# Optimization experiments

Measured on AMD Instinct MI355X. Metric: run time of the kernel, lower is better.

The kernel has to match this reference:

```python
import jax, jax.numpy as jnp
import numpy as np

EPS = 1e-5  # BatchNorm eps (eval mode, running stats mean=0, var=1)
BN_SCALE = 1.0 / np.sqrt(1.0 + EPS)


def setup_inputs() -> dict:
    key = jax.random.key(0)
    ks = jax.random.split(key, 5)
    N, T, C, V, K = 64, 300, 64, 25, 3
    x = jax.random.normal(ks[0], (N, T, C, V), dtype=jnp.float32)
    # G: Linear(T -> 2T, no bias), Linear(2T -> K, no bias)
    g_w1 = jax.random.normal(ks[1], (2 * T, T), dtype=jnp.float32) * (1.0 / np.sqrt(T))
    g_w2 = jax.random.normal(ks[2], (K, 2 * T), dtype=jnp.float32) * (1.0 / np.sqrt(2 * T))
    # L: Conv1d(C -> C//4, K, pad=K//2, no bias), Conv1d(C//4 -> C, 1, no bias)
    l_w1 = jax.random.normal(ks[3], (C // 4, C, K), dtype=jnp.float32) * (1.0 / np.sqrt(C * K))
    l_w2 = jax.random.normal(ks[4], (C, C // 4), dtype=jnp.float32) * (1.0 / np.sqrt(C // 4))
    return {"x": x, "g_w1": g_w1, "g_w2": g_w2, "l_w1": l_w1, "l_w2": l_w2}


def reference(x, g_w1, g_w2, l_w1, l_w2):
    # x: [N, T, C, V]; n_segment == T so n_batch == N
    N, T, C, V = x.shape
    K = g_w2.shape[0]
    pad = K // 2
    # new_x: [N, C, T, V]
    new_x = jnp.transpose(x, (0, 2, 1, 3))
    # adaptive avg pool over V -> [N, C, T]
    pooled = jnp.mean(new_x, axis=-1)

    # --- G branch: per-(n,c) temporal kernel of size K ---
    g_in = pooled.reshape(N * C, T)                         # [N*C, T]
    h = jnp.maximum(g_in @ g_w1.T * BN_SCALE, 0.0)          # Linear + BN(eval) + ReLU
    conv_kernel = jax.nn.softmax(h @ g_w2.T, axis=-1)       # [N*C, K]
    conv_kernel = conv_kernel.reshape(N, C, K)

    # --- L branch: local activation over time ---
    z = jax.lax.conv_general_dilated(
        pooled, l_w1, window_strides=(1,), padding=[(pad, pad)],
        dimension_numbers=("NCH", "OIH", "NCH"))              # [N, C//4, T]
    z = jnp.maximum(z * BN_SCALE, 0.0)
    local_act = jax.nn.sigmoid(jnp.einsum("nct,oc->not", z, l_w2))  # [N, C, T]

    new_x = new_x * local_act[..., None]                    # [N, C, T, V]

    # --- per-(n,c) depthwise temporal conv (groups = N*C) ---
    xpad = jnp.pad(new_x, ((0, 0), (0, 0), (pad, pad), (0, 0)))
    windows = jnp.stack([xpad[:, :, k:k + T, :] for k in range(K)], axis=-1)  # [N,C,T,V,K]
    out = jnp.einsum("nctvk,nck->nctv", windows, conv_kernel)

    return jnp.transpose(out, (0, 2, 1, 3))                 # [N, T, C, V]
```

## Files before the change

### kernel.cpp

```cpp
#include <hip/hip_runtime.h>
#include <hip/hip_bf16.h>
#include <math.h>

#define BN_SCALE_F 0.99999500003749969f

typedef short short8v __attribute__((ext_vector_type(8)));
typedef float float4v __attribute__((ext_vector_type(4)));


__global__ __launch_bounds__(256) void pool_kernel(const float* __restrict__ x,
                                                   float* __restrict__ pooledT) {
  __shared__ float buf[6400];
  int bid = blockIdx.x;
  const float4* src = (const float4*)(x + (size_t)bid * 6400);
  float4* b4 = (float4*)buf;
  for (int i = threadIdx.x; i < 1600; i += 256) b4[i] = src[i];
  __syncthreads();
  int wave = threadIdx.x >> 6;
  int c = threadIdx.x & 63;
  const float* p = buf + wave * 1600 + c * 25;
  float s = 0.f;
#pragma unroll
  for (int v = 0; v < 25; ++v) s += p[v];
  pooledT[(size_t)(bid * 4 + wave) * 64 + c] = s * 0.04f;
}

__global__ __launch_bounds__(256) void prep2_kernel(const float* __restrict__ pooledT,
                                                    const float* __restrict__ g_w1,
                                                    const float* __restrict__ l_w1,
                                                    __hip_bfloat16* __restrict__ pooledb,
                                                    __hip_bfloat16* __restrict__ w1b,
                                                    float* __restrict__ lw1r) {
  int bid = blockIdx.x;
  if (bid < 320) {
    __shared__ float tile[64][65];
    int n = bid / 5;
    int tt0 = (bid % 5) * 64;
    for (int i = threadIdx.x; i < 4096; i += 256) {
      int tt = i >> 6, c = i & 63;
      int t = tt0 + tt;
      tile[tt][c] = (t < 300) ? pooledT[((size_t)n * 300 + t) * 64 + c] : 0.f;
    }
    __syncthreads();
    for (int i = threadIdx.x; i < 4096; i += 256) {
      int c = i >> 6, tt = i & 63;
      pooledb[((size_t)(n * 64 + c)) * 320 + tt0 + tt] = __float2bfloat16(tile[tt][c]);
    }
  } else if (bid < 336) {
    int b = bid - 320;
    for (int i = b * 256 + threadIdx.x; i < 608 * 320; i += 16 * 256) {
      int j = i / 320, k = i - j * 320;
      float v = (j < 600 && k < 300) ? g_w1[(size_t)j * 300 + k] : 0.f;
      w1b[i] = __float2bfloat16(v);
    }
  } else {
    for (int i = threadIdx.x; i < 3072; i += 256) {
      int o = i / 192;
      int rem = i - o * 192;
      int c = rem / 3;
      int k = rem - c * 3;
      lw1r[c * 48 + o * 3 + k] = l_w1[i];
    }
  }
}

union GLSmem {
  struct {
    float hbuf[16][612];
    float logits[48];
  } g;
  struct {
    float p[64][81];
    float z[75][20];
  } l;
};

__global__ __launch_bounds__(320) void gl_kernel(const float* __restrict__ pooledT,
                                                 const __hip_bfloat16* __restrict__ pooledb,
                                                 const __hip_bfloat16* __restrict__ w1b,
                                                 const float* __restrict__ g_w2,
                                                 const float* __restrict__ lw1r,
                                                 const float* __restrict__ l_w2,
                                                 float* __restrict__ kern,
                                                 float* __restrict__ la) {
  __shared__ GLSmem sm;
  int bid = blockIdx.x;
  int tid = threadIdx.x;
  int wave = tid >> 6, lane = tid & 63;
  if (bid < 256) {
    int r0 = bid * 16;
    int row16 = lane & 15;
    int k8 = (lane >> 4) * 8;

    float4v acc[8];
#pragma unroll
    for (int q = 0; q < 8; ++q) acc[q] = (float4v){0.f, 0.f, 0.f, 0.f};

    const short* pa = (const short*)pooledb + (size_t)(r0 + row16) * 320 + k8;
    const short* pb = (const short*)w1b + k8;

    for (int kt = 0; kt < 10; ++kt) {
      short8v av = *(const short8v*)(pa + kt * 32);
#pragma unroll
      for (int q = 0; q < 8; ++q) {
        int jt = wave + 5 * q;
        if (jt < 38) {
          short8v bv = *(const short8v*)(pb + (size_t)(jt * 16 + row16) * 320 + kt * 32);
          acc[q] = __builtin_amdgcn_mfma_f32_16x16x32_bf16(av, bv, acc[q], 0, 0, 0);
        }
      }
    }

#pragma unroll
    for (int q = 0; q < 8; ++q) {
      int jt = wave + 5 * q;
      if (jt < 38) {
        int col = jt * 16 + row16;
#pragma unroll
        for (int reg = 0; reg < 4; ++reg) {
          int i = (lane >> 4) * 4 + reg;
          sm.g.hbuf[i][col] = fmaxf(acc[q][reg] * BN_SCALE_F, 0.f);
        }
      }
    }
    __syncthreads();

    for (int o = wave; o < 48; o += 5) {
      int r = o / 3, k = o - r * 3;
      float s = 0.f;
#pragma unroll
      for (int q = 0; q < 10; ++q) {
        int jj = lane + q * 64;
        if (jj < 600) s = fmaf(sm.g.hbuf[r][jj], g_w2[k * 600 + jj], s);
      }
#pragma unroll
      for (int off = 1; off < 64; off <<= 1) s += __shfl_xor(s, off, 64);
      if (lane == 0) sm.g.logits[o] = s;
    }
    __syncthreads();
    if (tid < 16) {
      float a = sm.g.logits[tid * 3 + 0];
      float b = sm.g.logits[tid * 3 + 1];
      float c = sm.g.logits[tid * 3 + 2];
      float m = fmaxf(a, fmaxf(b, c));
      float ea = expf(a - m), eb = expf(b - m), ec = expf(c - m);
      float inv = 1.f / (ea + eb + ec);
      size_t o = (size_t)(r0 + tid) * 3;
      kern[o] = ea * inv;
      kern[o + 1] = eb * inv;
      kern[o + 2] = ec * inv;
    }
  } else {
    int bid2 = bid - 256;
    int n = bid2 >> 2;
    int tc = bid2 & 3;
    int t0 = tc * 75;
    for (int i = tid; i < 77 * 64; i += 320) {
      int tt = i >> 6, c = i & 63;
      int gt = t0 - 1 + tt;
      sm.l.p[c][tt] = (gt >= 0 && gt < 300) ? pooledT[((size_t)n * 300 + gt) * 64 + c] : 0.f;
    }
    __syncthreads();
    if (tid < 256) {
      int og = __builtin_amdgcn_readfirstlane(tid >> 6);
      int tl = tid & 63;
      float acc[4] = {0.f, 0.f, 0.f, 0.f};
      const float* wb = lw1r + og * 12;
      for (int c = 0; c < 64; ++c) {
        const float* wr = wb + c * 48;
        float pk0 = sm.l.p[c][tl];
        float pk1 = sm.l.p[c][tl + 1];
        float pk2 = sm.l.p[c][tl + 2];
#pragma unroll
        for (int oi = 0; oi < 4; ++oi) {
          acc[oi] = fmaf(wr[oi * 3 + 0], pk0, acc[oi]);
          acc[oi] = fmaf(wr[oi * 3 + 1], pk1, acc[oi]);
          acc[oi] = fmaf(wr[oi * 3 + 2], pk2, acc[oi]);
        }
      }
      float4 zv;
      zv.x = fmaxf(acc[0] * BN_SCALE_F, 0.f);
      zv.y = fmaxf(acc[1] * BN_SCALE_F, 0.f);
      zv.z = fmaxf(acc[2] * BN_SCALE_F, 0.f);
      zv.w = fmaxf(acc[3] * BN_SCALE_F, 0.f);
      *(float4*)(&sm.l.z[tl][og * 4]) = zv;
    } else {
      int lane5 = tid - 256;
      int og = lane5 >> 4;
      int tlo = lane5 & 15;
      if (tlo < 11) {
        int tl = 64 + tlo;
        float acc[4] = {0.f, 0.f, 0.f, 0.f};
        for (int c = 0; c < 64; ++c) {
          const float* wr = lw1r + c * 48 + og * 12;
          float pk0 = sm.l.p[c][tl];
          float pk1 = sm.l.p[c][tl + 1];
          float pk2 = sm.l.p[c][tl + 2];
#pragma unroll
          for (int oi = 0; oi < 4; ++oi) {
            acc[oi] = fmaf(wr[oi * 3 + 0], pk0, acc[oi]);
            acc[oi] = fmaf(wr[oi * 3 + 1], pk1, acc[oi]);
            acc[oi] = fmaf(wr[oi * 3 + 2], pk2, acc[oi]);
          }
        }
        float4 zv;
        zv.x = fmaxf(acc[0] * BN_SCALE_F, 0.f);
        zv.y = fmaxf(acc[1] * BN_SCALE_F, 0.f);
        zv.z = fmaxf(acc[2] * BN_SCALE_F, 0.f);
        zv.w = fmaxf(acc[3] * BN_SCALE_F, 0.f);
        *(float4*)(&sm.l.z[tl][og * 4]) = zv;
      }
    }
    __syncthreads();
    {
      int c = tid / 5;
      int ts = tid - c * 5;
      const float4* w2v = (const float4*)(l_w2 + c * 16);
      float4 wA = w2v[0], wB = w2v[1], wC = w2v[2], wD = w2v[3];
      float* outp = la + (size_t)(n * 64 + c) * 300 + t0;
      for (int it = 0; it < 15; ++it) {
        int tl = ts + it * 5;
        const float4* zv = (const float4*)(&sm.l.z[tl][0]);
        float4 zA = zv[0], zB = zv[1], zC = zv[2], zD = zv[3];
        float s = zA.x * wA.x + zA.y * wA.y + zA.z * wA.z + zA.w * wA.w;
        s += zB.x * wB.x + zB.y * wB.y + zB.z * wB.z + zB.w * wB.w;
        s += zC.x * wC.x + zC.y * wC.y + zC.z * wC.z + zC.w * wC.w;
        s += zD.x * wD.x + zD.y * wD.y + zD.z * wD.z + zD.w * wD.w;
        outp[tl] = 1.f / (1.f + expf(-s));
      }
    }
  }
}

__global__ __launch_bounds__(256) void tam_final_kernel(const float* __restrict__ x,
                                                        const float* __restrict__ la,
                                                        const float* __restrict__ kern,
                                                        float* __restrict__ out) {
  int bid = blockIdx.x;
  int n = bid >> 4;
  int rem = bid & 15;
  int tch = rem >> 1;
  int half = rem & 1;
  int cv4 = half * 256 + threadIdx.x;
  if (cv4 >= 400) return;
  int e0 = cv4 * 4;
  int c0 = e0 / 25;
  int c3 = (e0 + 3) / 25;
  bool s1 = ((e0 + 1) / 25) != c0;
  bool s2 = ((e0 + 2) / 25) != c0;
  bool s3 = (c3 != c0);
  const float* lap0 = la + (size_t)(n * 64 + c0) * 300;
  const float* lap1 = la + (size_t)(n * 64 + c3) * 300;
  const float* kp0 = kern + (size_t)(n * 64 + c0) * 3;
  const float* kp1 = kern + (size_t)(n * 64 + c3) * 3;
  float k00 = kp0[0], k01 = kp0[1], k02 = kp0[2];
  float k10 = kp1[0], k11 = kp1[1], k12 = kp1[2];
  float4 K0 = {k00, s1 ? k10 : k00, s2 ? k10 : k00, s3 ? k10 : k00};
  float4 K1 = {k01, s1 ? k11 : k01, s2 ? k11 : k01, s3 ? k11 : k01};
  float4 K2 = {k02, s1 ? k12 : k02, s2 ? k12 : k02, s3 ? k12 : k02};

  const float4* xp = (const float4*)(x + (size_t)n * 480000) + cv4;
  float4* op = (float4*)(out + (size_t)n * 480000) + cv4;

  int t0 = tch * 38;
  int tend = t0 + 38;
  if (tend > 300) tend = 300;

#define LAMUL(dst, t)                                        \
  {                                                          \
    float l0 = lap0[(t)];                                    \
    float l1 = lap1[(t)];                                    \
    float4 xv = xp[(size_t)(t) * 400];                       \
    dst.x = xv.x * l0;                                       \
    dst.y = xv.y * (s1 ? l1 : l0);                           \
    dst.z = xv.z * (s2 ? l1 : l0);                           \
    dst.w = xv.w * (s3 ? l1 : l0);                           \
  }

  float4 am, ac, an;
  if (t0 > 0) {
    LAMUL(am, t0 - 1);
  } else {
    am = {0.f, 0.f, 0.f, 0.f};
  }
  LAMUL(ac, t0);
  for (int t = t0; t < tend; ++t) {
    if (t + 1 < 300) {
      LAMUL(an, t + 1);
    } else {
      an = {0.f, 0.f, 0.f, 0.f};
    }
    float4 o;
    o.x = fmaf(am.x, K0.x, fmaf(ac.x, K1.x, an.x * K2.x));
    o.y = fmaf(am.y, K0.y, fmaf(ac.y, K1.y, an.y * K2.y));
    o.z = fmaf(am.z, K0.z, fmaf(ac.z, K1.z, an.z * K2.z));
    o.w = fmaf(am.w, K0.w, fmaf(ac.w, K1.w, an.w * K2.w));
    op[(size_t)t * 400] = o;
    am = ac;
    ac = an;
  }
#undef LAMUL
}

extern "C" void kernel_launch(void* const* d_in, const int* in_sizes, int n_in,
                              void* d_out, int out_size, void* d_ws, size_t ws_size,
                              hipStream_t stream) {
  const float* x = (const float*)d_in[0];
  const float* g_w1 = (const float*)d_in[1];
  const float* g_w2 = (const float*)d_in[2];
  const float* l_w1 = (const float*)d_in[3];
  const float* l_w2 = (const float*)d_in[4];
  float* out = (float*)d_out;
  float* ws = (float*)d_ws;
  float* pooledT = ws;
  float* kern = ws + 1228800;
  float* lact = ws + 1228800 + 12288;
  __hip_bfloat16* pooledb = (__hip_bfloat16*)(ws + 2469888);
  __hip_bfloat16* w1b = (__hip_bfloat16*)(ws + 2469888 + 655360);
  float* lw1r = ws + 2469888 + 655360 + 97280;

  hipLaunchKernelGGL(pool_kernel, dim3(4800), dim3(256), 0, stream, x, pooledT);
  hipLaunchKernelGGL(prep2_kernel, dim3(337), dim3(256), 0, stream, pooledT, g_w1, l_w1,
                     pooledb, w1b, lw1r);
  hipLaunchKernelGGL(gl_kernel, dim3(512), dim3(320), 0, stream, pooledT, pooledb, w1b,
                     g_w2, lw1r, l_w2, kern, lact);
  hipLaunchKernelGGL(tam_final_kernel, dim3(1024), dim3(256), 0, stream, x, lact, kern, out);
}
```

Before: 107.7 us.

## Fuse weight prep into pool kernel and transpose pooled tile in gl_kernel LDS

```diff
diff --git a/kernel.cpp b/kernel.cpp
--- a/kernel.cpp
+++ b/kernel.cpp
@@ -9,45 +9,27 @@
 
 
 __global__ __launch_bounds__(256) void pool_kernel(const float* __restrict__ x,
-                                                   float* __restrict__ pooledT) {
+                                                   const float* __restrict__ g_w1,
+                                                   const float* __restrict__ l_w1,
+                                                   float* __restrict__ pooledT,
+                                                   __hip_bfloat16* __restrict__ w1b,
+                                                   float* __restrict__ lw1r) {
   __shared__ float buf[6400];
   int bid = blockIdx.x;
-  const float4* src = (const float4*)(x + (size_t)bid * 6400);
-  float4* b4 = (float4*)buf;
-  for (int i = threadIdx.x; i < 1600; i += 256) b4[i] = src[i];
-  __syncthreads();
-  int wave = threadIdx.x >> 6;
-  int c = threadIdx.x & 63;
-  const float* p = buf + wave * 1600 + c * 25;
-  float s = 0.f;
-#pragma unroll
-  for (int v = 0; v < 25; ++v) s += p[v];
-  pooledT[(size_t)(bid * 4 + wave) * 64 + c] = s * 0.04f;
-}
-
-__global__ __launch_bounds__(256) void prep2_kernel(const float* __restrict__ pooledT,
-                                                    const float* __restrict__ g_w1,
-                                                    const float* __restrict__ l_w1,
-                                                    __hip_bfloat16* __restrict__ pooledb,
-                                                    __hip_bfloat16* __restrict__ w1b,
-                                                    float* __restrict__ lw1r) {
-  int bid = blockIdx.x;
-  if (bid < 320) {
-    __shared__ float tile[64][65];
-    int n = bid / 5;
-    int tt0 = (bid % 5) * 64;
-    for (int i = threadIdx.x; i < 4096; i += 256) {
-      int tt = i >> 6, c = i & 63;
-      int t = tt0 + tt;
-      tile[tt][c] = (t < 300) ? pooledT[((size_t)n * 300 + t) * 64 + c] : 0.f;
-    }
-    __syncthreads();
-    for (int i = threadIdx.x; i < 4096; i += 256) {
-      int c = i >> 6, tt = i & 63;
-      pooledb[((size_t)(n * 64 + c)) * 320 + tt0 + tt] = __float2bfloat16(tile[tt][c]);
-    }
-  } else if (bid < 336) {
-    int b = bid - 320;
+  if (bid < 4800) {
+    const float4* src = (const float4*)(x + (size_t)bid * 6400);
+    float4* b4 = (float4*)buf;
+    for (int i = threadIdx.x; i < 1600; i += 256) b4[i] = src[i];
+    __syncthreads();
+    int wave = threadIdx.x >> 6;
+    int c = threadIdx.x & 63;
+    const float* p = buf + wave * 1600 + c * 25;
+    float s = 0.f;
+#pragma unroll
+    for (int v = 0; v < 25; ++v) s += p[v];
+    pooledT[(size_t)(bid * 4 + wave) * 64 + c] = s * 0.04f;
+  } else if (bid < 4816) {
+    int b = bid - 4800;
     for (int i = b * 256 + threadIdx.x; i < 608 * 320; i += 16 * 256) {
       int j = i / 320, k = i - j * 320;
       float v = (j < 600 && k < 300) ? g_w1[(size_t)j * 300 + k] : 0.f;
@@ -66,7 +48,8 @@
 
 union GLSmem {
   struct {
-    float hbuf[16][612];
+    __hip_bfloat16 abuf[16][328];
+    __hip_bfloat16 hbuf[16][612];
     float logits[48];
   } g;
   struct {
@@ -76,7 +59,6 @@
 };
 
 __global__ __launch_bounds__(320) void gl_kernel(const float* __restrict__ pooledT,
-                                                 const __hip_bfloat16* __restrict__ pooledb,
                                                  const __hip_bfloat16* __restrict__ w1b,
                                                  const float* __restrict__ g_w2,
                                                  const float* __restrict__ lw1r,
@@ -89,6 +71,16 @@
   int wave = tid >> 6, lane = tid & 63;
   if (bid < 256) {
     int r0 = bid * 16;
+    int n = bid >> 2;
+    int c0 = (bid & 3) * 16;
+    for (int i = tid; i < 5120; i += 320) {
+      int tt = i >> 4;
+      int cc = i & 15;
+      float v = (tt < 300) ? pooledT[((size_t)n * 300 + tt) * 64 + c0 + cc] : 0.f;
+      sm.g.abuf[cc][tt] = __float2bfloat16(v);
+    }
+    __syncthreads();
+
     int row16 = lane & 15;
     int k8 = (lane >> 4) * 8;
 
@@ -96,8 +88,8 @@
 #pragma unroll
     for (int q = 0; q < 8; ++q) acc[q] = (float4v){0.f, 0.f, 0.f, 0.f};
 
-    const short* pa = (const short*)pooledb + (size_t)(r0 + row16) * 320 + k8;
     const short* pb = (const short*)w1b + k8;
+    const short* pa = (const short*)&sm.g.abuf[row16][k8];
 
     for (int kt = 0; kt < 10; ++kt) {
       short8v av = *(const short8v*)(pa + kt * 32);
@@ -119,7 +111,7 @@
 #pragma unroll
         for (int reg = 0; reg < 4; ++reg) {
           int i = (lane >> 4) * 4 + reg;
-          sm.g.hbuf[i][col] = fmaxf(acc[q][reg] * BN_SCALE_F, 0.f);
+          sm.g.hbuf[i][col] = __float2bfloat16(fmaxf(acc[q][reg] * BN_SCALE_F, 0.f));
         }
       }
     }
@@ -131,7 +123,7 @@
 #pragma unroll
       for (int q = 0; q < 10; ++q) {
         int jj = lane + q * 64;
-        if (jj < 600) s = fmaf(sm.g.hbuf[r][jj], g_w2[k * 600 + jj], s);
+        if (jj < 600) s = fmaf(__bfloat162float(sm.g.hbuf[r][jj]), g_w2[k * 600 + jj], s);
       }
 #pragma unroll
       for (int off = 1; off < 64; off <<= 1) s += __shfl_xor(s, off, 64);
@@ -315,14 +307,12 @@
   float* pooledT = ws;
   float* kern = ws + 1228800;
   float* lact = ws + 1228800 + 12288;
-  __hip_bfloat16* pooledb = (__hip_bfloat16*)(ws + 2469888);
-  __hip_bfloat16* w1b = (__hip_bfloat16*)(ws + 2469888 + 655360);
-  float* lw1r = ws + 2469888 + 655360 + 97280;
-
-  hipLaunchKernelGGL(pool_kernel, dim3(4800), dim3(256), 0, stream, x, pooledT);
-  hipLaunchKernelGGL(prep2_kernel, dim3(337), dim3(256), 0, stream, pooledT, g_w1, l_w1,
-                     pooledb, w1b, lw1r);
-  hipLaunchKernelGGL(gl_kernel, dim3(512), dim3(320), 0, stream, pooledT, pooledb, w1b,
+  __hip_bfloat16* w1b = (__hip_bfloat16*)(ws + 2469888);
+  float* lw1r = ws + 2469888 + 97280;
+
+  hipLaunchKernelGGL(pool_kernel, dim3(4817), dim3(256), 0, stream, x, g_w1, l_w1,
+                     pooledT, w1b, lw1r);
+  hipLaunchKernelGGL(gl_kernel, dim3(512), dim3(320), 0, stream, pooledT, w1b,
                      g_w2, lw1r, l_w2, kern, lact);
   hipLaunchKernelGGL(tam_final_kernel, dim3(1024), dim3(256), 0, stream, x, lact, kern, out);
 }
```

After: 106.8 us. No clear change (-0.8%).
